# Performance work log

Hardware: AMD Instinct MI355X
Metric: run time of the kernel (lower is better)

## Reference

```python
import jax, jax.numpy as jnp
import numpy as np

N, E, G, H, C, DIN, DE = 20000, 320000, 32, 8, 56, 32, 5
HC = H * C  # 448
NEG_SLOPE = 0.2
EPS_BN = 1e-5


def _seg_softmax(scores, seg, num):
    # scores: [E, H], softmax over edges sharing the same target node
    m = jax.ops.segment_max(scores, seg, num_segments=num)
    e = jnp.exp(scores - m[seg])
    s = jax.ops.segment_sum(e, seg, num_segments=num)
    return e / (s[seg] + 1e-16)


def _add_self_loops(src, dst, eattr, n):
    # PyG fill_value='mean': self-loop edge_attr = mean of incoming edge_attr
    deg = jax.ops.segment_sum(jnp.ones((src.shape[0],), eattr.dtype), dst, num_segments=n)
    esum = jax.ops.segment_sum(eattr, dst, num_segments=n)
    loop_attr = esum / jnp.maximum(deg, 1.0)[:, None]
    ar = jnp.arange(n, dtype=src.dtype)
    return (jnp.concatenate([src, ar]), jnp.concatenate([dst, ar]),
            jnp.concatenate([eattr, loop_attr], axis=0))


def _gatv2(x, src, dst, eattr, Wl, Wr, We, att, bias, n):
    xl = (x @ Wl).reshape(n, H, C)  # source transform (messages)
    xr = (x @ Wr).reshape(n, H, C)  # target transform
    ee = (eattr @ We).reshape(-1, H, C)
    s = jax.nn.leaky_relu(xl[src] + xr[dst] + ee, NEG_SLOPE)  # [E, H, C]
    score = jnp.einsum('ehc,hc->eh', s, att)
    alpha = _seg_softmax(score, dst, n)
    out = jax.ops.segment_sum(alpha[..., None] * xl[src], dst, num_segments=n)
    return out.reshape(n, HC) + bias


def _bn(x, gamma, beta):
    m = x.mean(axis=0)
    v = x.var(axis=0)  # biased variance, as torch BatchNorm1d (training)
    return (x - m) * jax.lax.rsqrt(v + EPS_BN) * gamma + beta


def setup_inputs() -> dict:
    key = jax.random.key(0)
    ks = jax.random.split(key, 18)
    sc = lambda k, shape: (jax.random.normal(k, shape, jnp.float32) * 0.05)
    return {
        'x': jax.random.normal(ks[0], (N, DIN), jnp.float32),
        'edge_index': jax.random.randint(ks[1], (2, E), 0, N),
        'edge_attr': jax.random.normal(ks[2], (E, DE), jnp.float32),
        'batch': jnp.sort(jax.random.randint(ks[3], (N,), 0, G)),
        'Wl1': sc(ks[4], (DIN, HC)), 'Wr1': sc(ks[5], (DIN, HC)),
        'We1': sc(ks[6], (DE, HC)), 'att1': sc(ks[7], (H, C)),
        'bias1': jnp.zeros((HC,), jnp.float32),
        'Wl2': sc(ks[8], (HC, HC)), 'Wr2': sc(ks[9], (HC, HC)),
        'We2': sc(ks[10], (DE, HC)), 'att2': sc(ks[11], (H, C)),
        'bias2': jnp.zeros((HC,), jnp.float32),
        'bn_gamma': jnp.ones((HC,), jnp.float32),
        'bn_beta': jnp.zeros((HC,), jnp.float32),
        'Wlin': sc(ks[12], (HC, 18)),
        'blin': jnp.zeros((18,), jnp.float32),
    }


def reference(x, edge_index, edge_attr, batch, Wl1, Wr1, We1, att1, bias1,
              Wl2, Wr2, We2, att2, bias2, bn_gamma, bn_beta, Wlin, blin):
    src, dst = edge_index[0], edge_index[1]
    src2, dst2, ea2 = _add_self_loops(src, dst, edge_attr, N)
    # dropout is identity in eval
    h = _gatv2(x, src2, dst2, ea2, Wl1, Wr1, We1, att1, bias1, N)
    h = jax.nn.elu(h)
    h = _bn(h, bn_gamma, bn_beta)
    h = _gatv2(h, src2, dst2, ea2, Wl2, Wr2, We2, att2, bias2, N)
    # global mean pool per graph
    cnt = jax.ops.segment_sum(jnp.ones((N,), h.dtype), batch, num_segments=G)
    pooled = jax.ops.segment_sum(h, batch, num_segments=G) / jnp.maximum(cnt, 1.0)[:, None]
    pooled = _bn(pooled, bn_gamma, bn_beta)
    logits = pooled @ Wlin + blin
    return jax.nn.log_softmax(logits, axis=1)
```

## Files before the change

kernel.cpp:

```cpp
#include <hip/hip_runtime.h>
#include <hip/hip_bf16.h>

#define NN   20000
#define EE   320000
#define EN   340000
#define HH   8
#define CC   56
#define HC   448
#define SS   896
#define DEA  5
#define EAS  8
#define DINN 32
#define GG   32
#define NEG  0.2f

#define MT   157
#define NT   7

typedef short bf16x8 __attribute__((ext_vector_type(8)));
typedef float f32x4  __attribute__((ext_vector_type(4)));

static __device__ __forceinline__ unsigned short f2bf(float f) {
  unsigned int u = __float_as_uint(f);
  u += 0x7fffu + ((u >> 16) & 1u);
  return (unsigned short)(u >> 16);
}

static __device__ __forceinline__ f32x4 bf4_to_f32x4(uint2 r) {
  f32x4 o;
  o.x = __uint_as_float(r.x << 16);
  o.y = __uint_as_float(r.x & 0xffff0000u);
  o.z = __uint_as_float(r.y << 16);
  o.w = __uint_as_float(r.y & 0xffff0000u);
  return o;
}

__global__ void k_deg(const int* __restrict__ dst, int* deg) {
  int e = blockIdx.x * 256 + threadIdx.x;
  if (e < EE) atomicAdd(&deg[dst[e]], 1);
}

__global__ __launch_bounds__(1024) void k_scan(const int* __restrict__ deg, int* offs,
                                               int* cursor) {
  __shared__ int tot[1024];
  int t = threadIdx.x;
  int base = t * 20;
  int loc[20];
  int s = 0;
  #pragma unroll
  for (int i = 0; i < 20; i++) {
    int idx = base + i;
    int v = (idx < NN) ? deg[idx] + 1 : 0;
    loc[i] = s;
    s += v;
  }
  tot[t] = s;
  __syncthreads();
  for (int o = 1; o < 1024; o <<= 1) {
    int v = (t >= o) ? tot[t - o] : 0;
    __syncthreads();
    tot[t] += v;
    __syncthreads();
  }
  int basesum = (t == 0) ? 0 : tot[t - 1];
  #pragma unroll
  for (int i = 0; i < 20; i++) {
    int idx = base + i;
    if (idx < NN) { offs[idx] = basesum + loc[i]; cursor[idx] = basesum + loc[i]; }
  }
  if (t == 1023) offs[NN] = tot[1023];
}

__global__ void k_scatter(const int* __restrict__ src, const int* __restrict__ dst,
                          const float* __restrict__ ea,
                          int* cursor, int* __restrict__ csr_src, float* __restrict__ csr_ea) {
  int i = blockIdx.x * 256 + threadIdx.x;
  if (i >= EE) return;
  int d = dst[i], s = src[i];
  float a[DEA];
  #pragma unroll
  for (int j = 0; j < DEA; j++) a[j] = ea[(size_t)i * DEA + j];
  int pos = atomicAdd(&cursor[d], 1);
  csr_src[pos] = s;
  float* o = csr_ea + (size_t)pos * EAS;
  #pragma unroll
  for (int j = 0; j < DEA; j++) o[j] = a[j];
}

#define XCN (NN * DINN)
#define W1N (SS * DINN)
#define W2N (SS * HC)
__global__ void k_aux(const int* __restrict__ offs,
                      int* __restrict__ csr_src, float* __restrict__ csr_ea,
                      const float* __restrict__ x, unsigned short* __restrict__ xb,
                      const float* __restrict__ Wl1, const float* __restrict__ Wr1,
                      unsigned short* __restrict__ W1t,
                      const float* __restrict__ Wl2, const float* __restrict__ Wr2,
                      unsigned short* __restrict__ W2t) {
  int i = blockIdx.x * 256 + threadIdx.x;
  if (i < NN) {
    int n = i;
    int e0 = offs[n], e1 = offs[n + 1] - 1;
    float a0 = 0.f, a1 = 0.f, a2 = 0.f, a3 = 0.f, a4 = 0.f;
    for (int e = e0; e < e1; e++) {
      const float* p = csr_ea + (size_t)e * EAS;
      a0 += p[0]; a1 += p[1]; a2 += p[2]; a3 += p[3]; a4 += p[4];
    }
    float inv = 1.f / fmaxf((float)(e1 - e0), 1.f);
    csr_src[e1] = n;
    float* o = csr_ea + (size_t)e1 * EAS;
    o[0] = a0 * inv; o[1] = a1 * inv; o[2] = a2 * inv; o[3] = a3 * inv; o[4] = a4 * inv;
    return;
  }
  i -= NN;
  if (i < XCN) { xb[i] = f2bf(x[i]); return; }
  i -= XCN;
  if (i < W1N) {
    int k = i / SS, col = i - k * SS;
    int cc = (col < HC) ? col : col - HC;
    const float* W = (col < HC) ? Wl1 : Wr1;
    W1t[(size_t)col * DINN + k] = f2bf(W[(size_t)k * HC + cc]);
    return;
  }
  i -= W1N;
  if (i < W2N) {
    int k = i / SS, col = i - k * SS;
    int cc = (col < HC) ? col : col - HC;
    const float* W = (col < HC) ? Wl2 : Wr2;
    W2t[(size_t)col * HC + k] = f2bf(W[(size_t)k * HC + cc]);
  }
}

__global__ __launch_bounds__(256) void k_gemm1(const unsigned short* __restrict__ xb,
                                               const unsigned short* __restrict__ W1t,
                                               unsigned short* __restrict__ out) {
  int w = threadIdx.x >> 6, lane = threadIdx.x & 63;
  int q = lane >> 4, r = lane & 15;
  int m0 = (blockIdx.x * 4 + w) * 16;
  int n0 = blockIdx.y * 64;
  int arow = m0 + r; if (arow >= NN) arow = NN - 1;
  bf16x8 a = *(const bf16x8*)(xb + (size_t)arow * DINN + q * 8);
  #pragma unroll
  for (int j = 0; j < 4; j++) {
    bf16x8 b = *(const bf16x8*)(W1t + (size_t)(n0 + j * 16 + r) * DINN + q * 8);
    f32x4 acc = {0.f, 0.f, 0.f, 0.f};
    acc = __builtin_amdgcn_mfma_f32_16x16x32_bf16(a, b, acc, 0, 0, 0);
    #pragma unroll
    for (int reg = 0; reg < 4; reg++) {
      int row = m0 + q * 4 + reg;
      if (row < NN) out[(size_t)row * SS + n0 + j * 16 + r] = f2bf(acc[reg]);
    }
  }
}

__global__ __launch_bounds__(256) void k_attn(
    const unsigned short* __restrict__ xlr,
    const int* __restrict__ offs, const int* __restrict__ csr_src,
    const float* __restrict__ csr_ea,
    const float* __restrict__ We, const float* __restrict__ att,
    const float* __restrict__ bias, float* __restrict__ out, int apply_elu) {
  int wid = (blockIdx.x << 2) + (threadIdx.x >> 6);
  int n = wid >> 2;
  if (n >= NN) return;
  int hp = wid & 3;
  int lane = threadIdx.x & 63;
  int grp  = lane >> 5;
  int gl   = lane & 31;
  int hd   = gl >> 4;
  int sub  = gl & 15;
  bool cvalid = sub < 14;
  int cj = cvalid ? sub : 13;
  int cb = hp * 112 + hd * 56 + cj * 4;

  f32x4 xr4 = bf4_to_f32x4(*(const uint2*)(xlr + (size_t)n * SS + HC + cb));
  f32x4 at4 = *(const f32x4*)(att + cb);
  if (!cvalid) at4 = (f32x4){0.f, 0.f, 0.f, 0.f};
  f32x4 w0 = *(const f32x4*)(We + 0 * HC + cb);
  f32x4 w1 = *(const f32x4*)(We + 1 * HC + cb);
  f32x4 w2 = *(const f32x4*)(We + 2 * HC + cb);
  f32x4 w3 = *(const f32x4*)(We + 3 * HC + cb);
  f32x4 w4 = *(const f32x4*)(We + 4 * HC + cb);

  int e0 = offs[n], e1 = offs[n + 1];
  float l = 0.f;
  f32x4 acc = {0.f, 0.f, 0.f, 0.f};

  for (int e = e0 + grp; e < e1; e += 4) {
    int eb = e + 2;
    bool h2v = eb < e1;
    int ebc = h2v ? eb : e;
    int s0 = csr_src[e];
    int s1 = csr_src[ebc];
    const float* ep0 = csr_ea + (size_t)e * EAS;
    const float* ep1 = csr_ea + (size_t)ebc * EAS;
    f32x4 ea0 = *(const f32x4*)ep0;  float e40 = ep0[4];
    f32x4 ea1 = *(const f32x4*)ep1;  float e41 = ep1[4];
    uint2 r0 = *(const uint2*)(xlr + (size_t)s0 * SS + cb);
    uint2 r1 = *(const uint2*)(xlr + (size_t)s1 * SS + cb);
    f32x4 xl0 = bf4_to_f32x4(r0);
    f32x4 xl1 = bf4_to_f32x4(r1);

    f32x4 t0 = xl0 + xr4;
    t0 += ea0.x * w0; t0 += ea0.y * w1; t0 += ea0.z * w2; t0 += ea0.w * w3; t0 += e40 * w4;
    f32x4 t1 = xl1 + xr4;
    t1 += ea1.x * w0; t1 += ea1.y * w1; t1 += ea1.z * w2; t1 += ea1.w * w3; t1 += e41 * w4;
    t0.x = fmaxf(t0.x, NEG * t0.x); t0.y = fmaxf(t0.y, NEG * t0.y);
    t0.z = fmaxf(t0.z, NEG * t0.z); t0.w = fmaxf(t0.w, NEG * t0.w);
    t1.x = fmaxf(t1.x, NEG * t1.x); t1.y = fmaxf(t1.y, NEG * t1.y);
    t1.z = fmaxf(t1.z, NEG * t1.z); t1.w = fmaxf(t1.w, NEG * t1.w);
    float p0 = t0.x * at4.x + t0.y * at4.y + t0.z * at4.z + t0.w * at4.w;
    float p1 = t1.x * at4.x + t1.y * at4.y + t1.z * at4.z + t1.w * at4.w;
    p0 += __shfl_xor(p0, 1, 64);  p1 += __shfl_xor(p1, 1, 64);
    p0 += __shfl_xor(p0, 2, 64);  p1 += __shfl_xor(p1, 2, 64);
    p0 += __shfl_xor(p0, 4, 64);  p1 += __shfl_xor(p1, 4, 64);
    p0 += __shfl_xor(p0, 8, 64);  p1 += __shfl_xor(p1, 8, 64);
    float wv0 = __expf(fminf(p0, 60.f));
    float wv1 = h2v ? __expf(fminf(p1, 60.f)) : 0.f;
    acc += wv0 * xl0;
    acc += wv1 * xl1;
    l += wv0 + wv1;
  }
  l += __shfl_xor(l, 32, 64);
  acc.x += __shfl_xor(acc.x, 32, 64);
  acc.y += __shfl_xor(acc.y, 32, 64);
  acc.z += __shfl_xor(acc.z, 32, 64);
  acc.w += __shfl_xor(acc.w, 32, 64);

  if (lane < 32 && sub < 14) {
    f32x4 b4 = *(const f32x4*)(bias + cb);
    f32x4 o = acc * (1.f / (l + 1e-16f)) + b4;
    if (apply_elu) {
      o.x = o.x > 0.f ? o.x : (__expf(o.x) - 1.f);
      o.y = o.y > 0.f ? o.y : (__expf(o.y) - 1.f);
      o.z = o.z > 0.f ? o.z : (__expf(o.z) - 1.f);
      o.w = o.w > 0.f ? o.w : (__expf(o.w) - 1.f);
    }
    *(f32x4*)(out + (size_t)n * HC + cb) = o;
  }
}

__global__ __launch_bounds__(448) void k_bnstats(const float* __restrict__ h, float* stat) {
  int c = threadIdx.x;
  int rows_per = (NN + gridDim.x - 1) / gridDim.x;
  int r0 = blockIdx.x * rows_per, r1 = min(NN, r0 + rows_per);
  float s = 0.f, sq = 0.f;
  for (int r = r0; r < r1; r++) {
    float v = h[(size_t)r * HC + c];
    s += v; sq += v * v;
  }
  atomicAdd(&stat[c], s);
  atomicAdd(&stat[HC + c], sq);
}

__global__ void k_bnapply(const float* __restrict__ h, const float* __restrict__ stat,
                          const float* __restrict__ gam, const float* __restrict__ bet,
                          unsigned short* __restrict__ hA) {
  int i = blockIdx.x * 256 + threadIdx.x;
  if (i >= NN * HC) return;
  int c = i % HC;
  float mean = stat[c] * (1.f / NN);
  float var  = stat[HC + c] * (1.f / NN) - mean * mean;
  float sc = rsqrtf(var + 1e-5f) * gam[c];
  float sh = bet[c] - mean * sc;
  hA[i] = f2bf(h[i] * sc + sh);
}

__global__ __launch_bounds__(256) void k_gemm2(const unsigned short* __restrict__ A,
                                               const unsigned short* __restrict__ Bt,
                                               unsigned short* __restrict__ out) {
  __shared__ unsigned short As[128 * 64];
  __shared__ unsigned short Bs[128 * 64];
  int bid = blockIdx.x;
  int g = bid / 56, rem = bid - g * 56;
  int xs = min(8, MT - g * 8);
  int bx = g * 8 + rem % xs;
  int by = rem / xs;
  int t = threadIdx.x;
  int w = t >> 6, lane = t & 63;
  int wm = w >> 1, wn = w & 1;
  int q = lane >> 4, r = lane & 15;
  int m0 = bx * 128;
  int n0 = by * 128;

  const unsigned short *ag[4], *bg[4];
  unsigned short *la[4], *lb[4];
  #pragma unroll
  for (int j = 0; j < 4; j++) {
    int s = t + j * 256;
    int row = s >> 3, part = s & 7;
    int ar = m0 + row; if (ar >= NN) ar = NN - 1;
    ag[j] = A + (size_t)ar * HC + part * 8;
    bg[j] = Bt + (size_t)(n0 + row) * HC + part * 8;
    la[j] = As + s * 8;
    lb[j] = Bs + s * 8;
  }

  f32x4 zero = {0.f, 0.f, 0.f, 0.f};
  f32x4 acc[4][4];
  #pragma unroll
  for (int i = 0; i < 4; i++)
    #pragma unroll
    for (int j = 0; j < 4; j++) acc[i][j] = zero;

  for (int k0 = 0; k0 < HC; k0 += 64) {
    #pragma unroll
    for (int j = 0; j < 4; j++) {
      __builtin_amdgcn_global_load_lds(
          (const __attribute__((address_space(1))) unsigned int*)(ag[j] + k0),
          (__attribute__((address_space(3))) unsigned int*)la[j], 16, 0, 0);
      __builtin_amdgcn_global_load_lds(
          (const __attribute__((address_space(1))) unsigned int*)(bg[j] + k0),
          (__attribute__((address_space(3))) unsigned int*)lb[j], 16, 0, 0);
    }
    __syncthreads();
    #pragma unroll
    for (int kk = 0; kk < 64; kk += 32) {
      bf16x8 af[4], bf[4];
      #pragma unroll
      for (int i = 0; i < 4; i++)
        af[i] = *(const bf16x8*)(As + (wm * 64 + i * 16 + r) * 64 + kk + q * 8);
      #pragma unroll
      for (int j = 0; j < 4; j++)
        bf[j] = *(const bf16x8*)(Bs + (wn * 64 + j * 16 + r) * 64 + kk + q * 8);
      #pragma unroll
      for (int i = 0; i < 4; i++)
        #pragma unroll
        for (int j = 0; j < 4; j++)
          acc[i][j] = __builtin_amdgcn_mfma_f32_16x16x32_bf16(af[i], bf[j], acc[i][j], 0, 0, 0);
    }
    __syncthreads();
  }

  #pragma unroll
  for (int i = 0; i < 4; i++) {
    int row_base = m0 + wm * 64 + i * 16 + q * 4;
    #pragma unroll
    for (int j = 0; j < 4; j++) {
      int col = n0 + wn * 64 + j * 16 + r;
      #pragma unroll
      for (int reg = 0; reg < 4; reg++) {
        int row = row_base + reg;
        if (row < NN) out[(size_t)row * SS + col] = f2bf(acc[i][j][reg]);
      }
    }
  }
}

__global__ __launch_bounds__(448) void k_pool(const float* __restrict__ h2,
                                              const int* __restrict__ batch,
                                              float* pooled, int* cnt) {
  int c = threadIdx.x;
  int rows_per = (NN + gridDim.x - 1) / gridDim.x;
  int r0 = blockIdx.x * rows_per, r1 = min(NN, r0 + rows_per);
  if (r0 >= r1) return;
  float loc = 0.f;
  int rc = 0;
  int gcur = batch[r0];
  for (int r = r0; r < r1; r++) {
    int g = batch[r];
    if (g != gcur) {
      atomicAdd(&pooled[gcur * HC + c], loc);
      if (c == 0) atomicAdd(&cnt[gcur], rc);
      loc = 0.f; rc = 0; gcur = g;
    }
    loc += h2[(size_t)r * HC + c];
    rc++;
  }
  atomicAdd(&pooled[gcur * HC + c], loc);
  if (c == 0) atomicAdd(&cnt[gcur], rc);
}

__global__ __launch_bounds__(448) void k_final(const float* __restrict__ pooled_sum,
                                               const int* __restrict__ cnt,
                                               const float* __restrict__ gam,
                                               const float* __restrict__ bet,
                                               const float* __restrict__ Wlin,
                                               const float* __restrict__ blin,
                                               float* __restrict__ out) {
  __shared__ float P[GG * HC];
  __shared__ float L[GG * 18];
  __shared__ float red[GG];
  int c = threadIdx.x;
  float s = 0.f, sq = 0.f;
  for (int g = 0; g < GG; g++) {
    float v = pooled_sum[g * HC + c] / fmaxf((float)cnt[g], 1.f);
    P[g * HC + c] = v; s += v; sq += v * v;
  }
  float mean = s * (1.f / GG);
  float var  = sq * (1.f / GG) - mean * mean;
  float sc = rsqrtf(var + 1e-5f) * gam[c];
  float sh = bet[c] - mean * sc;
  for (int g = 0; g < GG; g++) P[g * HC + c] = P[g * HC + c] * sc + sh;
  __syncthreads();
  for (int o = c; o < GG * 18; o += HC) {
    int g = o / 18, j = o - g * 18;
    float acc = blin[j];
    for (int k = 0; k < HC; k++) acc += P[g * HC + k] * Wlin[k * 18 + j];
    L[o] = acc;
  }
  __syncthreads();
  if (c < GG) {
    float mx = -3.4e38f;
    for (int j = 0; j < 18; j++) mx = fmaxf(mx, L[c * 18 + j]);
    float se = 0.f;
    for (int j = 0; j < 18; j++) se += __expf(L[c * 18 + j] - mx);
    red[c] = mx + logf(se);
  }
  __syncthreads();
  for (int o = c; o < GG * 18; o += HC) out[o] = L[o] - red[o / 18];
}

extern "C" void kernel_launch(void* const* d_in, const int* in_sizes, int n_in,
                              void* d_out, int out_size, void* d_ws, size_t ws_size,
                              hipStream_t stream) {
  (void)in_sizes; (void)n_in; (void)out_size; (void)ws_size;
  const float* x     = (const float*)d_in[0];
  const int*   ei    = (const int*)d_in[1];
  const float* ea    = (const float*)d_in[2];
  const int*   batch = (const int*)d_in[3];
  const float* Wl1   = (const float*)d_in[4];
  const float* Wr1   = (const float*)d_in[5];
  const float* We1   = (const float*)d_in[6];
  const float* att1  = (const float*)d_in[7];
  const float* bias1 = (const float*)d_in[8];
  const float* Wl2   = (const float*)d_in[9];
  const float* Wr2   = (const float*)d_in[10];
  const float* We2   = (const float*)d_in[11];
  const float* att2  = (const float*)d_in[12];
  const float* bias2 = (const float*)d_in[13];
  const float* gam   = (const float*)d_in[14];
  const float* bet   = (const float*)d_in[15];
  const float* Wlin  = (const float*)d_in[16];
  const float* blin  = (const float*)d_in[17];
  float* out = (float*)d_out;
  const int* srcp = ei;
  const int* dstp = ei + EE;

  char* ws = (char*)d_ws;
  size_t off = 0;
  auto alloc = [&](size_t bytes) -> char* {
    char* p = ws + off;
    off = (off + bytes + 255) & ~(size_t)255;
    return p;
  };
  int*   deg     = (int*)  alloc(NN * 4);
  float* bnstat  = (float*)alloc(HC * 2 * 4);
  float* pooled  = (float*)alloc(GG * HC * 4 + GG * 4);
  int*   cnt     = (int*)(pooled + GG * HC);
  size_t zlen    = (size_t)((char*)(cnt + GG) - (char*)deg);

  int*   offs    = (int*)  alloc((NN + 1) * 4);
  int*   cursor  = (int*)  alloc(NN * 4);
  int*   csr_src = (int*)  alloc((size_t)EN * 4);
  float* csr_ea  = (float*)alloc((size_t)EN * EAS * 4);
  unsigned short* xlr = (unsigned short*)alloc((size_t)NN * SS * 2);
  float* h1      = (float*)alloc((size_t)NN * HC * 4);
  unsigned short* h1A = (unsigned short*)alloc((size_t)NN * HC * 2);
  unsigned short* xb  = (unsigned short*)alloc((size_t)NN * DINN * 2);
  unsigned short* W1t = (unsigned short*)alloc((size_t)SS * DINN * 2);
  unsigned short* W2t = (unsigned short*)alloc((size_t)SS * HC * 2);

  hipMemsetAsync(deg, 0, zlen, stream);
  k_deg<<<(EE + 255) / 256, 256, 0, stream>>>(dstp, deg);
  k_scan<<<1, 1024, 0, stream>>>(deg, offs, cursor);
  k_scatter<<<(EE + 255) / 256, 256, 0, stream>>>(srcp, dstp, ea, cursor, csr_src, csr_ea);
  k_aux<<<(NN + XCN + W1N + W2N + 255) / 256, 256, 0, stream>>>(
      offs, csr_src, csr_ea, x, xb, Wl1, Wr1, W1t, Wl2, Wr2, W2t);

  dim3 g1((NN + 63) / 64, SS / 64);
  k_gemm1<<<g1, 256, 0, stream>>>(xb, W1t, xlr);
  k_attn<<<NN, 256, 0, stream>>>(xlr, offs, csr_src, csr_ea, We1, att1, bias1, h1, 1);
  k_bnstats<<<256, HC, 0, stream>>>(h1, bnstat);
  k_bnapply<<<(NN * HC + 255) / 256, 256, 0, stream>>>(h1, bnstat, gam, bet, h1A);

  k_gemm2<<<MT * NT, 256, 0, stream>>>(h1A, W2t, xlr);
  k_attn<<<NN, 256, 0, stream>>>(xlr, offs, csr_src, csr_ea, We2, att2, bias2, h1, 0);

  k_pool<<<640, HC, 0, stream>>>(h1, batch, pooled, cnt);
  k_final<<<1, HC, 0, stream>>>(pooled, cnt, gam, bet, Wlin, blin, out);
}
```

Before: 492.7 us.

## Fold BatchNorm into GEMM2 weights and pad head layout for wide attention loads

Stops normalizing the layer-1 activations and instead folds the BatchNorm scale into the layer-2 weight matrix and the shift into a per-column GEMM bias. Layer-1 attention now writes ELU output directly as bf16, and BN statistics are read from that bf16 buffer. Features are stored with each 56-channel head padded to 64, so one wave handles a whole node with 16-byte gathers and no cross-half reduction. This removes the fp32 h1 write/read and the bnapply pass, at the cost of computing statistics from rounded values, a larger padded K in the GEMM, and larger padded buffers.

```diff
diff --git a/kernel.cpp b/kernel.cpp
--- a/kernel.cpp
+++ b/kernel.cpp
@@ -7,18 +7,21 @@
 #define HH   8
 #define CC   56
 #define HC   448
-#define SS   896
 #define DEA  5
 #define EAS  8
 #define DINN 32
 #define GG   32
 #define NEG  0.2f
 
+#define PS   512
+#define PSS  1024
 #define MT   157
 #define NT   7
+#define SS   896
 
 typedef short bf16x8 __attribute__((ext_vector_type(8)));
 typedef float f32x4  __attribute__((ext_vector_type(4)));
+typedef float f32x8  __attribute__((ext_vector_type(8)));
 
 static __device__ __forceinline__ unsigned short f2bf(float f) {
   unsigned int u = __float_as_uint(f);
@@ -26,12 +29,12 @@
   return (unsigned short)(u >> 16);
 }
 
-static __device__ __forceinline__ f32x4 bf4_to_f32x4(uint2 r) {
-  f32x4 o;
-  o.x = __uint_as_float(r.x << 16);
-  o.y = __uint_as_float(r.x & 0xffff0000u);
-  o.z = __uint_as_float(r.y << 16);
-  o.w = __uint_as_float(r.y & 0xffff0000u);
+static __device__ __forceinline__ f32x8 bf8_to_f32x8(uint4 u) {
+  f32x8 o;
+  o[0] = __uint_as_float(u.x << 16); o[1] = __uint_as_float(u.x & 0xffff0000u);
+  o[2] = __uint_as_float(u.y << 16); o[3] = __uint_as_float(u.y & 0xffff0000u);
+  o[4] = __uint_as_float(u.z << 16); o[5] = __uint_as_float(u.z & 0xffff0000u);
+  o[6] = __uint_as_float(u.w << 16); o[7] = __uint_as_float(u.w & 0xffff0000u);
   return o;
 }
 
@@ -145,10 +148,12 @@
     bf16x8 b = *(const bf16x8*)(W1t + (size_t)(n0 + j * 16 + r) * DINN + q * 8);
     f32x4 acc = {0.f, 0.f, 0.f, 0.f};
     acc = __builtin_amdgcn_mfma_f32_16x16x32_bf16(a, b, acc, 0, 0, 0);
+    int col = n0 + j * 16 + r;
+    int cp = col + 8 * (col / 56);
     #pragma unroll
     for (int reg = 0; reg < 4; reg++) {
       int row = m0 + q * 4 + reg;
-      if (row < NN) out[(size_t)row * SS + n0 + j * 16 + r] = f2bf(acc[reg]);
+      if (row < NN) out[(size_t)row * PSS + cp] = f2bf(acc[reg]);
     }
   }
 }
@@ -158,35 +163,32 @@
     const int* __restrict__ offs, const int* __restrict__ csr_src,
     const float* __restrict__ csr_ea,
     const float* __restrict__ We, const float* __restrict__ att,
-    const float* __restrict__ bias, float* __restrict__ out, int apply_elu) {
-  int wid = (blockIdx.x << 2) + (threadIdx.x >> 6);
-  int n = wid >> 2;
+    const float* __restrict__ bias,
+    unsigned short* __restrict__ outb, float* __restrict__ outf, int layer1) {
+  int n = blockIdx.x * 4 + (threadIdx.x >> 6);
   if (n >= NN) return;
-  int hp = wid & 3;
   int lane = threadIdx.x & 63;
-  int grp  = lane >> 5;
-  int gl   = lane & 31;
-  int hd   = gl >> 4;
-  int sub  = gl & 15;
-  bool cvalid = sub < 14;
-  int cj = cvalid ? sub : 13;
-  int cb = hp * 112 + hd * 56 + cj * 4;
-
-  f32x4 xr4 = bf4_to_f32x4(*(const uint2*)(xlr + (size_t)n * SS + HC + cb));
-  f32x4 at4 = *(const f32x4*)(att + cb);
-  if (!cvalid) at4 = (f32x4){0.f, 0.f, 0.f, 0.f};
-  f32x4 w0 = *(const f32x4*)(We + 0 * HC + cb);
-  f32x4 w1 = *(const f32x4*)(We + 1 * HC + cb);
-  f32x4 w2 = *(const f32x4*)(We + 2 * HC + cb);
-  f32x4 w3 = *(const f32x4*)(We + 3 * HC + cb);
-  f32x4 w4 = *(const f32x4*)(We + 4 * HC + cb);
+  int head = lane >> 3, sub = lane & 7;
+  bool v = sub < 7;
+  int pc = head * 64 + sub * 8;
+  int cr = head * 56 + (v ? sub : 6) * 8;
+
+  f32x8 z = {0.f,0.f,0.f,0.f,0.f,0.f,0.f,0.f};
+  f32x8 xr = bf8_to_f32x8(*(const uint4*)(xlr + (size_t)n * PSS + PS + pc));
+  f32x8 at = *(const f32x8*)(att + cr);
+  if (!v) at = z;
+  f32x8 w0 = *(const f32x8*)(We + 0 * HC + cr);
+  f32x8 w1 = *(const f32x8*)(We + 1 * HC + cr);
+  f32x8 w2 = *(const f32x8*)(We + 2 * HC + cr);
+  f32x8 w3 = *(const f32x8*)(We + 3 * HC + cr);
+  f32x8 w4 = *(const f32x8*)(We + 4 * HC + cr);
 
   int e0 = offs[n], e1 = offs[n + 1];
   float l = 0.f;
-  f32x4 acc = {0.f, 0.f, 0.f, 0.f};
-
-  for (int e = e0 + grp; e < e1; e += 4) {
-    int eb = e + 2;
+  f32x8 acc = z;
+
+  for (int e = e0; e < e1; e += 2) {
+    int eb = e + 1;
     bool h2v = eb < e1;
     int ebc = h2v ? eb : e;
     int s0 = csr_src[e];
@@ -195,78 +197,98 @@
     const float* ep1 = csr_ea + (size_t)ebc * EAS;
     f32x4 ea0 = *(const f32x4*)ep0;  float e40 = ep0[4];
     f32x4 ea1 = *(const f32x4*)ep1;  float e41 = ep1[4];
-    uint2 r0 = *(const uint2*)(xlr + (size_t)s0 * SS + cb);
-    uint2 r1 = *(const uint2*)(xlr + (size_t)s1 * SS + cb);
-    f32x4 xl0 = bf4_to_f32x4(r0);
-    f32x4 xl1 = bf4_to_f32x4(r1);
-
-    f32x4 t0 = xl0 + xr4;
+    uint4 g0 = *(const uint4*)(xlr + (size_t)s0 * PSS + pc);
+    uint4 g1 = *(const uint4*)(xlr + (size_t)s1 * PSS + pc);
+    f32x8 xl0 = bf8_to_f32x8(g0);
+    f32x8 xl1 = bf8_to_f32x8(g1);
+
+    f32x8 t0 = xl0 + xr;
     t0 += ea0.x * w0; t0 += ea0.y * w1; t0 += ea0.z * w2; t0 += ea0.w * w3; t0 += e40 * w4;
-    f32x4 t1 = xl1 + xr4;
+    f32x8 t1 = xl1 + xr;
     t1 += ea1.x * w0; t1 += ea1.y * w1; t1 += ea1.z * w2; t1 += ea1.w * w3; t1 += e41 * w4;
-    t0.x = fmaxf(t0.x, NEG * t0.x); t0.y = fmaxf(t0.y, NEG * t0.y);
-    t0.z = fmaxf(t0.z, NEG * t0.z); t0.w = fmaxf(t0.w, NEG * t0.w);
-    t1.x = fmaxf(t1.x, NEG * t1.x); t1.y = fmaxf(t1.y, NEG * t1.y);
-    t1.z = fmaxf(t1.z, NEG * t1.z); t1.w = fmaxf(t1.w, NEG * t1.w);
-    float p0 = t0.x * at4.x + t0.y * at4.y + t0.z * at4.z + t0.w * at4.w;
-    float p1 = t1.x * at4.x + t1.y * at4.y + t1.z * at4.z + t1.w * at4.w;
+    #pragma unroll
+    for (int i = 0; i < 8; i++) {
+      t0[i] = fmaxf(t0[i], NEG * t0[i]);
+      t1[i] = fmaxf(t1[i], NEG * t1[i]);
+    }
+    float p0 = 0.f, p1 = 0.f;
+    #pragma unroll
+    for (int i = 0; i < 8; i++) { p0 += t0[i] * at[i]; p1 += t1[i] * at[i]; }
     p0 += __shfl_xor(p0, 1, 64);  p1 += __shfl_xor(p1, 1, 64);
     p0 += __shfl_xor(p0, 2, 64);  p1 += __shfl_xor(p1, 2, 64);
     p0 += __shfl_xor(p0, 4, 64);  p1 += __shfl_xor(p1, 4, 64);
-    p0 += __shfl_xor(p0, 8, 64);  p1 += __shfl_xor(p1, 8, 64);
     float wv0 = __expf(fminf(p0, 60.f));
     float wv1 = h2v ? __expf(fminf(p1, 60.f)) : 0.f;
     acc += wv0 * xl0;
     acc += wv1 * xl1;
     l += wv0 + wv1;
   }
-  l += __shfl_xor(l, 32, 64);
-  acc.x += __shfl_xor(acc.x, 32, 64);
-  acc.y += __shfl_xor(acc.y, 32, 64);
-  acc.z += __shfl_xor(acc.z, 32, 64);
-  acc.w += __shfl_xor(acc.w, 32, 64);
-
-  if (lane < 32 && sub < 14) {
-    f32x4 b4 = *(const f32x4*)(bias + cb);
-    f32x4 o = acc * (1.f / (l + 1e-16f)) + b4;
-    if (apply_elu) {
-      o.x = o.x > 0.f ? o.x : (__expf(o.x) - 1.f);
-      o.y = o.y > 0.f ? o.y : (__expf(o.y) - 1.f);
-      o.z = o.z > 0.f ? o.z : (__expf(o.z) - 1.f);
-      o.w = o.w > 0.f ? o.w : (__expf(o.w) - 1.f);
-    }
-    *(f32x4*)(out + (size_t)n * HC + cb) = o;
-  }
-}
-
-__global__ __launch_bounds__(448) void k_bnstats(const float* __restrict__ h, float* stat) {
+
+  f32x8 b8 = *(const f32x8*)(bias + cr);
+  f32x8 o = acc * (1.f / (l + 1e-16f)) + b8;
+  if (layer1) {
+    #pragma unroll
+    for (int i = 0; i < 8; i++) o[i] = o[i] > 0.f ? o[i] : (__expf(o[i]) - 1.f);
+    uint4 pk;
+    pk.x = ((unsigned int)f2bf(o[1]) << 16) | f2bf(o[0]);
+    pk.y = ((unsigned int)f2bf(o[3]) << 16) | f2bf(o[2]);
+    pk.z = ((unsigned int)f2bf(o[5]) << 16) | f2bf(o[4]);
+    pk.w = ((unsigned int)f2bf(o[7]) << 16) | f2bf(o[6]);
+    if (!v) pk = (uint4){0u, 0u, 0u, 0u};
+    *(uint4*)(outb + (size_t)n * PS + pc) = pk;
+  } else if (v) {
+    float* dst = outf + (size_t)n * HC + cr;
+    *(f32x4*)dst       = (f32x4){o[0], o[1], o[2], o[3]};
+    *(f32x4*)(dst + 4) = (f32x4){o[4], o[5], o[6], o[7]};
+  }
+}
+
+__global__ __launch_bounds__(448) void k_bnstats(const unsigned short* __restrict__ h,
+                                                 float* stat) {
   int c = threadIdx.x;
+  int cp = c + 8 * (c / 56);
   int rows_per = (NN + gridDim.x - 1) / gridDim.x;
   int r0 = blockIdx.x * rows_per, r1 = min(NN, r0 + rows_per);
   float s = 0.f, sq = 0.f;
   for (int r = r0; r < r1; r++) {
-    float v = h[(size_t)r * HC + c];
+    unsigned int u = h[(size_t)r * PS + cp];
+    float v = __uint_as_float(u << 16);
     s += v; sq += v * v;
   }
   atomicAdd(&stat[c], s);
   atomicAdd(&stat[HC + c], sq);
 }
 
-__global__ void k_bnapply(const float* __restrict__ h, const float* __restrict__ stat,
-                          const float* __restrict__ gam, const float* __restrict__ bet,
-                          unsigned short* __restrict__ hA) {
-  int i = blockIdx.x * 256 + threadIdx.x;
-  if (i >= NN * HC) return;
-  int c = i % HC;
-  float mean = stat[c] * (1.f / NN);
-  float var  = stat[HC + c] * (1.f / NN) - mean * mean;
-  float sc = rsqrtf(var + 1e-5f) * gam[c];
-  float sh = bet[c] - mean * sc;
-  hA[i] = f2bf(h[i] * sc + sh);
+__global__ __launch_bounds__(64) void k_w2fix(const unsigned short* __restrict__ W2t,
+                                              const float* __restrict__ stat,
+                                              const float* __restrict__ gam,
+                                              const float* __restrict__ bet,
+                                              unsigned short* __restrict__ W2s,
+                                              float* __restrict__ bias2) {
+  int j = blockIdx.x;
+  int t = threadIdx.x;
+  float bacc = 0.f;
+  #pragma unroll
+  for (int it = 0; it < 7; it++) {
+    int k = t + it * 64;
+    float w = __uint_as_float((unsigned int)W2t[(size_t)j * HC + k] << 16);
+    float mean = stat[k] * (1.f / NN);
+    float var  = stat[HC + k] * (1.f / NN) - mean * mean;
+    float sc = rsqrtf(var + 1e-5f) * gam[k];
+    float sh = bet[k] - mean * sc;
+    bacc += sh * w;
+    int kp = k + 8 * (k / 56);
+    W2s[(size_t)j * PS + kp] = f2bf(sc * w);
+  }
+  W2s[(size_t)j * PS + (t >> 3) * 64 + 56 + (t & 7)] = 0;
+  #pragma unroll
+  for (int m = 32; m >= 1; m >>= 1) bacc += __shfl_xor(bacc, m, 64);
+  if (t == 0) bias2[j] = bacc;
 }
 
 __global__ __launch_bounds__(256) void k_gemm2(const unsigned short* __restrict__ A,
                                                const unsigned short* __restrict__ Bt,
+                                               const float* __restrict__ bias2,
                                                unsigned short* __restrict__ out) {
   __shared__ unsigned short As[128 * 64];
   __shared__ unsigned short Bs[128 * 64];
@@ -289,8 +311,8 @@
     int s = t + j * 256;
     int row = s >> 3, part = s & 7;
     int ar = m0 + row; if (ar >= NN) ar = NN - 1;
-    ag[j] = A + (size_t)ar * HC + part * 8;
-    bg[j] = Bt + (size_t)(n0 + row) * HC + part * 8;
+    ag[j] = A + (size_t)ar * PS + part * 8;
+    bg[j] = Bt + (size_t)(n0 + row) * PS + part * 8;
     la[j] = As + s * 8;
     lb[j] = Bs + s * 8;
   }
@@ -302,7 +324,7 @@
     #pragma unroll
     for (int j = 0; j < 4; j++) acc[i][j] = zero;
 
-  for (int k0 = 0; k0 < HC; k0 += 64) {
+  for (int k0 = 0; k0 < PS; k0 += 64) {
     #pragma unroll
     for (int j = 0; j < 4; j++) {
       __builtin_amdgcn_global_load_lds(
@@ -332,15 +354,17 @@
   }
 
   #pragma unroll
-  for (int i = 0; i < 4; i++) {
-    int row_base = m0 + wm * 64 + i * 16 + q * 4;
-    #pragma unroll
-    for (int j = 0; j < 4; j++) {
-      int col = n0 + wn * 64 + j * 16 + r;
+  for (int j = 0; j < 4; j++) {
+    int col = n0 + wn * 64 + j * 16 + r;
+    int cp = col + 8 * (col / 56);
+    float bs = bias2[col];
+    #pragma unroll
+    for (int i = 0; i < 4; i++) {
+      int row_base = m0 + wm * 64 + i * 16 + q * 4;
       #pragma unroll
       for (int reg = 0; reg < 4; reg++) {
         int row = row_base + reg;
-        if (row < NN) out[(size_t)row * SS + col] = f2bf(acc[i][j][reg]);
+        if (row < NN) out[(size_t)row * PSS + cp] = f2bf(acc[i][j][reg] + bs);
       }
     }
   }
@@ -427,7 +451,7 @@
   const float* Wr2   = (const float*)d_in[10];
   const float* We2   = (const float*)d_in[11];
   const float* att2  = (const float*)d_in[12];
-  const float* bias2 = (const float*)d_in[13];
+  const float* bias2in = (const float*)d_in[13];
   const float* gam   = (const float*)d_in[14];
   const float* bet   = (const float*)d_in[15];
   const float* Wlin  = (const float*)d_in[16];
@@ -453,12 +477,14 @@
   int*   cursor  = (int*)  alloc(NN * 4);
   int*   csr_src = (int*)  alloc((size_t)EN * 4);
   float* csr_ea  = (float*)alloc((size_t)EN * EAS * 4);
-  unsigned short* xlr = (unsigned short*)alloc((size_t)NN * SS * 2);
-  float* h1      = (float*)alloc((size_t)NN * HC * 4);
-  unsigned short* h1A = (unsigned short*)alloc((size_t)NN * HC * 2);
+  unsigned short* xlr = (unsigned short*)alloc((size_t)NN * PSS * 2);
+  unsigned short* h1b = (unsigned short*)alloc((size_t)NN * PS * 2);
+  float* h1f     = (float*)alloc((size_t)NN * HC * 4);
   unsigned short* xb  = (unsigned short*)alloc((size_t)NN * DINN * 2);
   unsigned short* W1t = (unsigned short*)alloc((size_t)SS * DINN * 2);
   unsigned short* W2t = (unsigned short*)alloc((size_t)SS * HC * 2);
+  unsigned short* W2s = (unsigned short*)alloc((size_t)SS * PS * 2);
+  float* bias2   = (float*)alloc(SS * 4);
 
   hipMemsetAsync(deg, 0, zlen, stream);
   k_deg<<<(EE + 255) / 256, 256, 0, stream>>>(dstp, deg);
@@ -469,13 +495,15 @@
 
   dim3 g1((NN + 63) / 64, SS / 64);
   k_gemm1<<<g1, 256, 0, stream>>>(xb, W1t, xlr);
-  k_attn<<<NN, 256, 0, stream>>>(xlr, offs, csr_src, csr_ea, We1, att1, bias1, h1, 1);
-  k_bnstats<<<256, HC, 0, stream>>>(h1, bnstat);
-  k_bnapply<<<(NN * HC + 255) / 256, 256, 0, stream>>>(h1, bnstat, gam, bet, h1A);
-
-  k_gemm2<<<MT * NT, 256, 0, stream>>>(h1A, W2t, xlr);
-  k_attn<<<NN, 256, 0, stream>>>(xlr, offs, csr_src, csr_ea, We2, att2, bias2, h1, 0);
-
-  k_pool<<<640, HC, 0, stream>>>(h1, batch, pooled, cnt);
+  k_attn<<<(NN + 3) / 4, 256, 0, stream>>>(xlr, offs, csr_src, csr_ea,
+                                           We1, att1, bias1, h1b, h1f, 1);
+  k_bnstats<<<256, HC, 0, stream>>>(h1b, bnstat);
+  k_w2fix<<<SS, 64, 0, stream>>>(W2t, bnstat, gam, bet, W2s, bias2);
+
+  k_gemm2<<<MT * NT, 256, 0, stream>>>(h1b, W2s, bias2, xlr);
+  k_attn<<<(NN + 3) / 4, 256, 0, stream>>>(xlr, offs, csr_src, csr_ea,
+                                           We2, att2, bias2in, h1b, h1f, 0);
+
+  k_pool<<<640, HC, 0, stream>>>(h1f, batch, pooled, cnt);
   k_final<<<1, HC, 0, stream>>>(pooled, cnt, gam, bet, Wlin, blin, out);
 }
```

Result: faster. 473.9 us (-3.8%).
